# Optimization experiments

Measured on AMD Instinct MI355X. Metric: run time of the kernel, lower is better.

Reference implementation:

```python
import jax, jax.numpy as jnp
import numpy as np

B, T, H = 16, 2048, 1024

def setup_inputs() -> dict:
    key = jax.random.key(0)
    k1, k2, k3, k4 = jax.random.split(key, 4)
    stdv = 1.0 / np.sqrt(H)
    return {
        "hidden": jax.random.normal(k1, (B, H), dtype=jnp.float32),
        "encoder_outputs": jax.random.normal(k2, (B, T, 2 * H), dtype=jnp.float32),
        "W": jax.random.normal(k3, (H, 3 * H), dtype=jnp.float32) * stdv,  # nn.Linear(3H, H) weight
        "b": jnp.zeros((H,), dtype=jnp.float32),
        "v": jax.random.normal(k4, (H,), dtype=jnp.float32) * stdv,
    }

def reference(hidden, encoder_outputs, W, b, v):
    # hidden: (B,H); encoder_outputs: (B,T,2H)
    Bsz, Tlen, _ = encoder_outputs.shape
    Hrep = jnp.broadcast_to(hidden[:, None, :], (Bsz, Tlen, hidden.shape[-1]))  # (B,T,H)
    cat = jnp.concatenate([Hrep, encoder_outputs], axis=2)                      # (B,T,3H)
    energy = jnp.tanh(jnp.einsum('btk,hk->bth', cat, W) + b)                    # (B,T,H)
    scores = jnp.einsum('bth,h->bt', energy, v)[:, None, :]                     # (B,1,T), == bmm(v, energy^T)
    return jax.nn.softmax(scores, axis=2)
```

## Files before the change

### kernel.cpp

```cpp
#include <hip/hip_runtime.h>
#include <cstdint>

#define B_SZ 16
#define T_SZ 2048
#define H_SZ 1024
#define K_SZ 2048
#define M_SZ (B_SZ * T_SZ)

#define BM 128
#define BN 128
#define BK 64
#define LDK 72
#define KTILES (K_SZ / BK)

typedef _Float16 half8_t __attribute__((ext_vector_type(8)));
typedef float float4_t __attribute__((ext_vector_type(4)));

__device__ __forceinline__ void glds16(const _Float16* g, _Float16* l) {
    __builtin_amdgcn_global_load_lds(
        (const __attribute__((address_space(1))) void*)g,
        (__attribute__((address_space(3))) void*)l, 16, 0, 0);
}

__global__ __launch_bounds__(256) void cvt_enc_kernel(
    const float* __restrict__ src, _Float16* __restrict__ dst) {
    size_t i = ((size_t)blockIdx.x * 256 + threadIdx.x) * 8;
    float4_t a = *(const float4_t*)(src + i);
    float4_t b = *(const float4_t*)(src + i + 4);
    half8_t h;
    h[0] = (_Float16)a[0]; h[1] = (_Float16)a[1];
    h[2] = (_Float16)a[2]; h[3] = (_Float16)a[3];
    h[4] = (_Float16)b[0]; h[5] = (_Float16)b[1];
    h[6] = (_Float16)b[2]; h[7] = (_Float16)b[3];
    *(half8_t*)(dst + i) = h;
}

__global__ __launch_bounds__(256) void cvt_w2_kernel(
    const float* __restrict__ W, _Float16* __restrict__ dst) {
    int idx8 = blockIdx.x * 256 + threadIdx.x;
    int n = idx8 >> 8, k8 = (idx8 & 255) * 8;
    const float* src = W + (size_t)n * 3072 + H_SZ + k8;
    float4_t a = *(const float4_t*)(src);
    float4_t b = *(const float4_t*)(src + 4);
    half8_t h;
    h[0] = (_Float16)a[0]; h[1] = (_Float16)a[1];
    h[2] = (_Float16)a[2]; h[3] = (_Float16)a[3];
    h[4] = (_Float16)b[0]; h[5] = (_Float16)b[1];
    h[6] = (_Float16)b[2]; h[7] = (_Float16)b[3];
    *(half8_t*)(dst + (size_t)n * K_SZ + k8) = h;
}

__global__ __launch_bounds__(256) void hpart_kernel(
    const float* __restrict__ hidden, const float* __restrict__ W,
    const float* __restrict__ bias, float* __restrict__ hpart) {
    int wave = (blockIdx.x * 256 + threadIdx.x) >> 6;
    int lane = threadIdx.x & 63;
    int b = wave >> 10;
    int h = wave & 1023;
    const float* wrow = W + (size_t)h * 3072;
    const float* hrow = hidden + b * H_SZ;
    int k0 = lane * 16;
    float acc = 0.f;
#pragma unroll
    for (int j = 0; j < 4; ++j) {
        float4_t wv = *(const float4_t*)(wrow + k0 + j * 4);
        float4_t hv = *(const float4_t*)(hrow + k0 + j * 4);
        acc += wv[0] * hv[0] + wv[1] * hv[1] + wv[2] * hv[2] + wv[3] * hv[3];
    }
#pragma unroll
    for (int off = 32; off >= 1; off >>= 1) acc += __shfl_xor(acc, off, 64);
    if (lane == 0) hpart[b * H_SZ + h] = acc + bias[h];
}

__global__ __launch_bounds__(256, 4) void attn_gemm16_kernel(
    const _Float16* __restrict__ A, const _Float16* __restrict__ Bm,
    const float* __restrict__ hpart, const float* __restrict__ v,
    float* __restrict__ partial) {
    __shared__ _Float16 Af[BM * BK];
    __shared__ _Float16 Bf[BN * BK];
    __shared__ float hp_s[BN];
    __shared__ float v_s[BN];

    const int bidx = blockIdx.x;
    const int blockN = bidx & 7;
    const int blockM = bidx >> 3;
    const int tid = threadIdx.x;
    const int lane = tid & 63;
    const int w = tid >> 6;
    const int wm = w & 1, wn = w >> 1;
    const int m16 = lane & 15, quad = lane >> 4;
    const int sw = m16 & 7;

    const int n0 = blockN * BN;
    const int batch = blockM >> 4;

    if (tid < BN) {
        hp_s[tid] = hpart[batch * H_SZ + n0 + tid];
        v_s[tid] = v[n0 + tid];
    }

    float4_t acc[4][4];
#pragma unroll
    for (int i = 0; i < 4; ++i)
#pragma unroll
        for (int j = 0; j < 4; ++j) acc[i][j] = (float4_t){0.f, 0.f, 0.f, 0.f};

    const _Float16* Abase = A + (size_t)(blockM * BM) * K_SZ;
    const _Float16* Bbase = Bm + (size_t)n0 * K_SZ;

    const int r_s = tid >> 3;
    const int jcol = (((tid & 7) ^ ((tid >> 3) & 7))) * 8;

    for (int kt = 0; kt < KTILES; ++kt) {
        __syncthreads();
        const _Float16* As = Abase + kt * BK + jcol;
        const _Float16* Bs = Bbase + kt * BK + jcol;
#pragma unroll
        for (int i = 0; i < 4; ++i) {
            int slot = i * 256 + tid;
            glds16(As + (size_t)(r_s + i * 32) * K_SZ, &Af[slot * 8]);
        }
#pragma unroll
        for (int i = 0; i < 4; ++i) {
            int slot = i * 256 + tid;
            glds16(Bs + (size_t)(r_s + i * 32) * K_SZ, &Bf[slot * 8]);
        }
        __syncthreads();
#pragma unroll
        for (int ks = 0; ks < 2; ++ks) {
            half8_t afrag[4], bfrag[4];
#pragma unroll
            for (int tm = 0; tm < 4; ++tm) {
                int r = wm * 64 + tm * 16 + m16;
                int p = ((ks * 4 + quad) ^ sw) * 8;
                afrag[tm] = *(const half8_t*)&Af[r * BK + p];
            }
#pragma unroll
            for (int tn = 0; tn < 4; ++tn) {
                int r = wn * 64 + tn * 16 + m16;
                int p = ((ks * 4 + quad) ^ sw) * 8;
                bfrag[tn] = *(const half8_t*)&Bf[r * BK + p];
            }
#pragma unroll
            for (int tm = 0; tm < 4; ++tm)
#pragma unroll
                for (int tn = 0; tn < 4; ++tn)
                    acc[tm][tn] = __builtin_amdgcn_mfma_f32_16x16x32_f16(
                        afrag[tm], bfrag[tn], acc[tm][tn], 0, 0, 0);
        }
    }

    const int slice = blockN * 2 + wn;
#pragma unroll
    for (int tm = 0; tm < 4; ++tm) {
        float s0 = 0.f, s1 = 0.f, s2 = 0.f, s3 = 0.f;
#pragma unroll
        for (int tn = 0; tn < 4; ++tn) {
            int nl = wn * 64 + tn * 16 + m16;
            float hpv = hp_s[nl];
            float vv = v_s[nl];
            s0 += tanhf(acc[tm][tn][0] + hpv) * vv;
            s1 += tanhf(acc[tm][tn][1] + hpv) * vv;
            s2 += tanhf(acc[tm][tn][2] + hpv) * vv;
            s3 += tanhf(acc[tm][tn][3] + hpv) * vv;
        }
#pragma unroll
        for (int off = 1; off < 16; off <<= 1) {
            s0 += __shfl_xor(s0, off, 64);
            s1 += __shfl_xor(s1, off, 64);
            s2 += __shfl_xor(s2, off, 64);
            s3 += __shfl_xor(s3, off, 64);
        }
        if (m16 == 0) {
            int gm = blockM * BM + wm * 64 + tm * 16 + quad * 4;
            float* dst = partial + (size_t)slice * M_SZ + gm;
            dst[0] = s0; dst[1] = s1; dst[2] = s2; dst[3] = s3;
        }
    }
}

__global__ __launch_bounds__(256, 2) void attn_gemm_kernel(
    const float* __restrict__ enc, const float* __restrict__ W,
    const float* __restrict__ hpart, const float* __restrict__ v,
    float* __restrict__ partial) {
    __shared__ _Float16 Af[BM * LDK];
    __shared__ _Float16 Bf[BN * LDK];
    __shared__ float hp_s[BN];
    __shared__ float v_s[BN];

    const int bidx = blockIdx.x;
    const int blockN = bidx & 7;
    const int blockM = bidx >> 3;
    const int tid = threadIdx.x;
    const int lane = tid & 63;
    const int w = tid >> 6;
    const int wm = w & 1, wn = w >> 1;
    const int m16 = lane & 15, quad = lane >> 4;

    const int n0 = blockN * BN;
    const int batch = blockM >> 4;

    if (tid < BN) {
        hp_s[tid] = hpart[batch * H_SZ + n0 + tid];
        v_s[tid] = v[n0 + tid];
    }

    float4_t acc[4][4];
#pragma unroll
    for (int i = 0; i < 4; ++i)
#pragma unroll
        for (int j = 0; j < 4; ++j) acc[i][j] = (float4_t){0.f, 0.f, 0.f, 0.f};

    const float* Abase = enc + (size_t)(blockM * BM) * K_SZ;
    const float* Bbase = W + (size_t)n0 * 3072 + H_SZ;

    for (int kt = 0; kt < KTILES; ++kt) {
        __syncthreads();
        const float* Asrc0 = Abase + kt * BK;
#pragma unroll
        for (int i = 0; i < 4; ++i) {
            int f8 = i * 256 + tid;
            int r = f8 >> 3, c8 = f8 & 7;
            const float* src = Asrc0 + (size_t)r * K_SZ + c8 * 8;
            float4_t lo = *(const float4_t*)(src);
            float4_t hi = *(const float4_t*)(src + 4);
            half8_t hv;
            hv[0] = (_Float16)lo[0]; hv[1] = (_Float16)lo[1];
            hv[2] = (_Float16)lo[2]; hv[3] = (_Float16)lo[3];
            hv[4] = (_Float16)hi[0]; hv[5] = (_Float16)hi[1];
            hv[6] = (_Float16)hi[2]; hv[7] = (_Float16)hi[3];
            *(half8_t*)&Af[r * LDK + c8 * 8] = hv;
        }
        const float* Bsrc0 = Bbase + kt * BK;
#pragma unroll
        for (int i = 0; i < 4; ++i) {
            int f8 = i * 256 + tid;
            int r = f8 >> 3, c8 = f8 & 7;
            const float* src = Bsrc0 + (size_t)r * 3072 + c8 * 8;
            float4_t lo = *(const float4_t*)(src);
            float4_t hi = *(const float4_t*)(src + 4);
            half8_t hv;
            hv[0] = (_Float16)lo[0]; hv[1] = (_Float16)lo[1];
            hv[2] = (_Float16)lo[2]; hv[3] = (_Float16)lo[3];
            hv[4] = (_Float16)hi[0]; hv[5] = (_Float16)hi[1];
            hv[6] = (_Float16)hi[2]; hv[7] = (_Float16)hi[3];
            *(half8_t*)&Bf[r * LDK + c8 * 8] = hv;
        }
        __syncthreads();
#pragma unroll
        for (int ks = 0; ks < 2; ++ks) {
            half8_t afrag[4], bfrag[4];
#pragma unroll
            for (int tm = 0; tm < 4; ++tm)
                afrag[tm] = *(const half8_t*)&Af[(wm * 64 + tm * 16 + m16) * LDK + ks * 32 + quad * 8];
#pragma unroll
            for (int tn = 0; tn < 4; ++tn)
                bfrag[tn] = *(const half8_t*)&Bf[(wn * 64 + tn * 16 + m16) * LDK + ks * 32 + quad * 8];
#pragma unroll
            for (int tm = 0; tm < 4; ++tm)
#pragma unroll
                for (int tn = 0; tn < 4; ++tn)
                    acc[tm][tn] = __builtin_amdgcn_mfma_f32_16x16x32_f16(
                        afrag[tm], bfrag[tn], acc[tm][tn], 0, 0, 0);
        }
    }

    const int slice = blockN * 2 + wn;
#pragma unroll
    for (int tm = 0; tm < 4; ++tm) {
        float s0 = 0.f, s1 = 0.f, s2 = 0.f, s3 = 0.f;
#pragma unroll
        for (int tn = 0; tn < 4; ++tn) {
            int nl = wn * 64 + tn * 16 + m16;
            float hpv = hp_s[nl];
            float vv = v_s[nl];
            s0 += tanhf(acc[tm][tn][0] + hpv) * vv;
            s1 += tanhf(acc[tm][tn][1] + hpv) * vv;
            s2 += tanhf(acc[tm][tn][2] + hpv) * vv;
            s3 += tanhf(acc[tm][tn][3] + hpv) * vv;
        }
#pragma unroll
        for (int off = 1; off < 16; off <<= 1) {
            s0 += __shfl_xor(s0, off, 64);
            s1 += __shfl_xor(s1, off, 64);
            s2 += __shfl_xor(s2, off, 64);
            s3 += __shfl_xor(s3, off, 64);
        }
        if (m16 == 0) {
            int gm = blockM * BM + wm * 64 + tm * 16 + quad * 4;
            float* dst = partial + (size_t)slice * M_SZ + gm;
            dst[0] = s0; dst[1] = s1; dst[2] = s2; dst[3] = s3;
        }
    }
}

__global__ __launch_bounds__(256) void softmax_kernel(
    const float* __restrict__ partial, float* __restrict__ out) {
    __shared__ float red[256];
    const int b = blockIdx.x;
    const int tid = threadIdx.x;
    float sc[8];
    float mymax = -1e30f;
#pragma unroll
    for (int i = 0; i < 8; ++i) {
        int t = i * 256 + tid;
        float s = 0.f;
#pragma unroll
        for (int sl = 0; sl < 16; ++sl) s += partial[(size_t)sl * M_SZ + b * T_SZ + t];
        sc[i] = s;
        mymax = fmaxf(mymax, s);
    }
    red[tid] = mymax;
    __syncthreads();
    for (int off = 128; off >= 1; off >>= 1) {
        if (tid < off) red[tid] = fmaxf(red[tid], red[tid + off]);
        __syncthreads();
    }
    float mx = red[0];
    __syncthreads();
    float mysum = 0.f;
#pragma unroll
    for (int i = 0; i < 8; ++i) {
        sc[i] = expf(sc[i] - mx);
        mysum += sc[i];
    }
    red[tid] = mysum;
    __syncthreads();
    for (int off = 128; off >= 1; off >>= 1) {
        if (tid < off) red[tid] += red[tid + off];
        __syncthreads();
    }
    float inv = 1.0f / red[0];
#pragma unroll
    for (int i = 0; i < 8; ++i) out[b * T_SZ + i * 256 + tid] = sc[i] * inv;
}

extern "C" void kernel_launch(void* const* d_in, const int* in_sizes, int n_in,
                              void* d_out, int out_size, void* d_ws, size_t ws_size,
                              hipStream_t stream) {
    const float* hidden = (const float*)d_in[0];
    const float* enc    = (const float*)d_in[1];
    const float* W      = (const float*)d_in[2];
    const float* bias   = (const float*)d_in[3];
    const float* v      = (const float*)d_in[4];
    float* out = (float*)d_out;

    float* hpart   = (float*)d_ws;
    float* partial = hpart + B_SZ * H_SZ;
    _Float16* w2h  = (_Float16*)(partial + 16 * M_SZ);
    _Float16* e16  = w2h + (size_t)H_SZ * K_SZ;
    const size_t need = (size_t)((char*)(e16 + (size_t)M_SZ * K_SZ) - (char*)d_ws);

    hipLaunchKernelGGL(hpart_kernel, dim3(4096), dim3(256), 0, stream,
                       hidden, W, bias, hpart);
    if (ws_size >= need) {
        hipLaunchKernelGGL(cvt_enc_kernel, dim3(32768), dim3(256), 0, stream, enc, e16);
        hipLaunchKernelGGL(cvt_w2_kernel, dim3(1024), dim3(256), 0, stream, W, w2h);
        hipLaunchKernelGGL(attn_gemm16_kernel, dim3(2048), dim3(256), 0, stream,
                           e16, w2h, hpart, v, partial);
    } else {
        hipLaunchKernelGGL(attn_gemm_kernel, dim3(2048), dim3(256), 0, stream,
                           enc, W, hpart, v, partial);
    }
    hipLaunchKernelGGL(softmax_kernel, dim3(B_SZ), dim3(256), 0, stream,
                       partial, out);
}
```

Measured before the change: 566.5 us.

## Pre-pack W2 into MFMA fragment order and load B fragments directly from global

The fp16 conversion of W's encoder half now writes it in a packed layout matching the MFMA 16x16x32 B-fragment order. The GEMM kernel drops the B shared-memory tile and loads each wave's B fragments straight from global/L2 into registers with coalesced 16-byte loads. This removes the B LDS staging, its LDS reads and half the shared memory, but B is now re-read from cache by every wave pair with no LDS reuse. The loads are also issued between the barriers, which may expose global latency.

```diff
diff --git a/kernel.cpp b/kernel.cpp
--- a/kernel.cpp
+++ b/kernel.cpp
@@ -38,8 +38,8 @@
 __global__ __launch_bounds__(256) void cvt_w2_kernel(
     const float* __restrict__ W, _Float16* __restrict__ dst) {
     int idx8 = blockIdx.x * 256 + threadIdx.x;
-    int n = idx8 >> 8, k8 = (idx8 & 255) * 8;
-    const float* src = W + (size_t)n * 3072 + H_SZ + k8;
+    int n = idx8 >> 8, k = (idx8 & 255) * 8;
+    const float* src = W + (size_t)n * 3072 + H_SZ + k;
     float4_t a = *(const float4_t*)(src);
     float4_t b = *(const float4_t*)(src + 4);
     half8_t h;
@@ -47,7 +47,10 @@
     h[2] = (_Float16)a[2]; h[3] = (_Float16)a[3];
     h[4] = (_Float16)b[0]; h[5] = (_Float16)b[1];
     h[6] = (_Float16)b[2]; h[7] = (_Float16)b[3];
-    *(half8_t*)(dst + (size_t)n * K_SZ + k8) = h;
+    int nblk = n >> 4, m16 = n & 15;
+    int kblk = k >> 5, quad = (k >> 3) & 3;
+    size_t di = (((size_t)nblk * 64 + kblk) * 64 + quad * 16 + m16) * 8;
+    *(half8_t*)(dst + di) = h;
 }
 
 __global__ __launch_bounds__(256) void hpart_kernel(
@@ -73,11 +76,10 @@
 }
 
 __global__ __launch_bounds__(256, 4) void attn_gemm16_kernel(
-    const _Float16* __restrict__ A, const _Float16* __restrict__ Bm,
+    const _Float16* __restrict__ A, const _Float16* __restrict__ Bp,
     const float* __restrict__ hpart, const float* __restrict__ v,
     float* __restrict__ partial) {
     __shared__ _Float16 Af[BM * BK];
-    __shared__ _Float16 Bf[BN * BK];
     __shared__ float hp_s[BN];
     __shared__ float v_s[BN];
 
@@ -106,7 +108,7 @@
         for (int j = 0; j < 4; ++j) acc[i][j] = (float4_t){0.f, 0.f, 0.f, 0.f};
 
     const _Float16* Abase = A + (size_t)(blockM * BM) * K_SZ;
-    const _Float16* Bbase = Bm + (size_t)n0 * K_SZ;
+    const _Float16* Bfr = Bp + (((size_t)(blockN * 8 + wn * 4) * 64) * 64 + lane) * 8;
 
     const int r_s = tid >> 3;
     const int jcol = (((tid & 7) ^ ((tid >> 3) & 7))) * 8;
@@ -114,21 +116,22 @@
     for (int kt = 0; kt < KTILES; ++kt) {
         __syncthreads();
         const _Float16* As = Abase + kt * BK + jcol;
-        const _Float16* Bs = Bbase + kt * BK + jcol;
 #pragma unroll
         for (int i = 0; i < 4; ++i) {
             int slot = i * 256 + tid;
             glds16(As + (size_t)(r_s + i * 32) * K_SZ, &Af[slot * 8]);
         }
-#pragma unroll
-        for (int i = 0; i < 4; ++i) {
-            int slot = i * 256 + tid;
-            glds16(Bs + (size_t)(r_s + i * 32) * K_SZ, &Bf[slot * 8]);
-        }
+        half8_t bfrag[2][4];
+#pragma unroll
+        for (int ks = 0; ks < 2; ++ks)
+#pragma unroll
+            for (int tn = 0; tn < 4; ++tn)
+                bfrag[ks][tn] = *(const half8_t*)(
+                    Bfr + (size_t)tn * (64 * 64 * 8) + (size_t)(kt * 2 + ks) * (64 * 8));
         __syncthreads();
 #pragma unroll
         for (int ks = 0; ks < 2; ++ks) {
-            half8_t afrag[4], bfrag[4];
+            half8_t afrag[4];
 #pragma unroll
             for (int tm = 0; tm < 4; ++tm) {
                 int r = wm * 64 + tm * 16 + m16;
@@ -136,17 +139,11 @@
                 afrag[tm] = *(const half8_t*)&Af[r * BK + p];
             }
 #pragma unroll
-            for (int tn = 0; tn < 4; ++tn) {
-                int r = wn * 64 + tn * 16 + m16;
-                int p = ((ks * 4 + quad) ^ sw) * 8;
-                bfrag[tn] = *(const half8_t*)&Bf[r * BK + p];
-            }
-#pragma unroll
             for (int tm = 0; tm < 4; ++tm)
 #pragma unroll
                 for (int tn = 0; tn < 4; ++tn)
                     acc[tm][tn] = __builtin_amdgcn_mfma_f32_16x16x32_f16(
-                        afrag[tm], bfrag[tn], acc[tm][tn], 0, 0, 0);
+                        afrag[tm], bfrag[ks][tn], acc[tm][tn], 0, 0, 0);
         }
     }
 
```

Result: no change. 558.0 us (-1.5%).
